# Kernel tuning notes

Hardware: AMD Instinct MI355X
Metric: run time of the kernel (lower is better)

## Reference

```python
import jax, jax.numpy as jnp
import numpy as np

NUM_ITERATIONS = 3  # init kwarg num_iterations
EPS = 1e-12         # F.normalize eps


def _k_means_routing(priors, num_iterations):
    # priors: (B, O, I, J) = (batch, out_capsules, in_capsules, out_length)
    out = priors.mean(axis=-2, keepdims=True)  # (B, O, 1, J)
    for _ in range(num_iterations):
        norm = jnp.sqrt(jnp.sum(out * out, axis=-1, keepdims=True))
        out_n = out / jnp.maximum(norm, EPS)                       # L2 normalize over J
        logits = jnp.sum(priors * out_n, axis=-1, keepdims=True)   # (B, O, I, 1) dot similarity
        coef = jax.nn.softmax(logits, axis=-2)                     # softmax over in_capsules
        out = jnp.sum(coef * priors, axis=-2, keepdims=True)       # (B, O, 1, J)
    return jnp.squeeze(out, axis=-2)  # (B, O, J); squash=False so no squash


def setup_inputs() -> dict:
    key = jax.random.key(0)
    k1, k2 = jax.random.split(key)
    B, I, L = 32, 512, 64   # batch, in_capsules, in_length
    O, J = 128, 64          # out_capsules, out_length
    x = jax.random.normal(k1, (B, I, L), dtype=jnp.float32)
    # xavier_uniform for weight (O, J, L): fan_in = J*L... torch uses size(1)*prod(rest)
    bound = float(np.sqrt(6.0 / (J * L + O * L)))
    weight = jax.random.uniform(k2, (O, J, L), dtype=jnp.float32, minval=-bound, maxval=bound)
    return {"x": x, "weight": weight}


def reference(x, weight):
    # priors[b,o,i,j] = sum_l weight[o,j,l] * x[b,i,l]  -> (B, O, I, J)
    priors = jnp.einsum('ojl,bil->boij', weight, x)
    return _k_means_routing(priors, NUM_ITERATIONS)
```

## Files before the change

### kernel.cpp

```cpp
#include <hip/hip_runtime.h>
#include <hip/hip_fp16.h>


#define CB 32
#define CI 512
#define CL 64
#define CO 128
#define OPB 8
#define NT 1024

typedef _Float16 half8 __attribute__((ext_vector_type(8)));
typedef float f32x4 __attribute__((ext_vector_type(4)));

static __device__ __forceinline__ _Float16 half_sel(uint v, int sh) {
  union { unsigned short s; _Float16 h; } c;
  c.s = (unsigned short)(v >> sh);
  return c.h;
}

__global__ __launch_bounds__(256) void caps_gram(const float* __restrict__ wg,
                                                 __half2* __restrict__ Gq) {
  const int o = blockIdx.x;
  const int h = blockIdx.y;
  const int t = threadIdx.x;
  __shared__ float wl[64 * 65];
#pragma unroll
  for (int k = 0; k < 16; ++k) {
    int f = t + 256 * k;
    int j = f >> 6, l = f & 63;
    wl[j * 65 + l] = wg[(o << 12) + f];
  }
  __syncthreads();
  const int l1 = h * 32 + (t >> 3);
  const int kq = t & 7;
  const int l2b = kq << 3;
  float acc[8];
#pragma unroll
  for (int m = 0; m < 8; ++m) acc[m] = 0.f;
#pragma unroll 4
  for (int j = 0; j < 64; ++j) {
    float wa = wl[j * 65 + l1];
#pragma unroll
    for (int m = 0; m < 8; ++m) acc[m] += wa * wl[j * 65 + l2b + m];
  }
  union { __half2 h2[4]; uint4 u; } pk;
#pragma unroll
  for (int q = 0; q < 4; ++q)
    pk.h2[q] = __floats2half2_rn(acc[2 * q], acc[2 * q + 1]);
  reinterpret_cast<uint4*>(Gq)[(o << 9) + (kq << 6) + l1] = pk.u;
}

__global__ __launch_bounds__(NT)
__attribute__((amdgpu_num_vgpr(64)))
void caps_main(const float* __restrict__ xg,
               const float* __restrict__ wg,
               const __half2* __restrict__ Gq,
               float* __restrict__ outg) {
  const int b = blockIdx.y;
  const int obase = blockIdx.x * OPB;
  const int t = threadIdx.x;
  const int w = t >> 6;
  const int lane = t & 63;
  const int g = lane >> 4;
  const int o15 = lane & 15;
  const int oc = o15 & 7;

  __shared__ __align__(16) _Float16 xs[CI * CL];
  __shared__ __align__(16) _Float16 cfx[OPB * CI];
  __shared__ __align__(16) _Float16 wn16[OPB * CL];
  __shared__ __align__(16) float xc_s[OPB * CL];
  __shared__ float se_part[16 * OPB];
  float* const xcpart = reinterpret_cast<float*>(cfx);
  char* const xs_b = reinterpret_cast<char*>(xs);
  char* const cf_b = reinterpret_cast<char*>(cfx);
  char* const wn_b = reinterpret_cast<char*>(wn16);

  const int qh = w >> 2, nt = w & 3;
  const int lcol = nt * 16 + o15;

  const uint4* Gp = reinterpret_cast<const uint4*>(Gq) +
                    ((obase + (w & 7)) << 9) + lane;
  uint4 ga0, ga1;

  {
    const float4* xg4 = reinterpret_cast<const float4*>(xg + b * (CI * CL));
#pragma unroll
    for (int k = 0; k < 4; ++k) {
      int f = t + NT * k;
      int i = f >> 3, lu = f & 7;
      float4 a = xg4[2 * f];
      float4 c = xg4[2 * f + 1];
      union { _Float16 h[8]; uint4 u; } cv;
      cv.h[0] = (_Float16)a.x; cv.h[1] = (_Float16)a.y;
      cv.h[2] = (_Float16)a.z; cv.h[3] = (_Float16)a.w;
      cv.h[4] = (_Float16)c.x; cv.h[5] = (_Float16)c.y;
      cv.h[6] = (_Float16)c.z; cv.h[7] = (_Float16)c.w;
      int off = ((i >> 4) * 4 + (lu >> 1)) * 512 + (i & 15) * 32 + (lu & 1) * 16;
      *reinterpret_cast<uint4*>(xs_b + off) = cv.u;
    }
  }
  __syncthreads();

  uint4 bt0, bt1, bt2, bt3;
  float xbs = 0.f;
  {
    const uint* xrd32 = reinterpret_cast<const uint*>(
                            xs_b + nt * 512 + ((o15 & 8) << 1)) +
                        ((o15 & 7) >> 1);
    const int sh = (o15 & 1) << 4;
#define GATHW(K, BT)                                                        \
  {                                                                         \
    int P = qh * 16 + (K)*4 + g;                                            \
    const uint* xk = xrd32 + (P >> 1) * 512 + (P & 1) * 64;                 \
    uint d0 = xk[0], d1 = xk[8], d2 = xk[16], d3 = xk[24];                  \
    uint d4 = xk[32], d5 = xk[40], d6 = xk[48], d7 = xk[56];                \
    union { _Float16 h[8]; uint4 u; } fv;                                   \
    fv.h[0] = half_sel(d0, sh); fv.h[1] = half_sel(d1, sh);                 \
    fv.h[2] = half_sel(d2, sh); fv.h[3] = half_sel(d3, sh);                 \
    fv.h[4] = half_sel(d4, sh); fv.h[5] = half_sel(d5, sh);                 \
    fv.h[6] = half_sel(d6, sh); fv.h[7] = half_sel(d7, sh);                 \
    xbs += (float)fv.h[0] + (float)fv.h[1] + (float)fv.h[2] +               \
           (float)fv.h[3] + (float)fv.h[4] + (float)fv.h[5] +               \
           (float)fv.h[6] + (float)fv.h[7];                                 \
    BT = fv.u;                                                              \
  }
    GATHW(0, bt0) GATHW(1, bt1) GATHW(2, bt2) GATHW(3, bt3)
#undef GATHW
    xbs += __shfl_xor(xbs, 16, 64);
    xbs += __shfl_xor(xbs, 32, 64);
    if (g == 0) xcpart[qh * 512 + lcol] = xbs;
    if (w < 8) { ga0 = Gp[0]; ga1 = Gp[64]; }
  }
  __syncthreads();

  for (int pass = 0; pass < 4; ++pass) {
    if (pass > 0) {
      half8 bw0 = *reinterpret_cast<const half8*>(
          wn_b + oc * 128 + ((g ^ oc) << 4));
      half8 bw1 = *reinterpret_cast<const half8*>(
          wn_b + oc * 128 + (((4 + g) ^ oc) << 4));
      float sacc = 0.f;
#pragma unroll
      for (int ti = 0; ti < 2; ++ti) {
        const int st = 2 * w + ti;
        const int itb = st * 2048;
        const int abase = o15 * 32 + ((g & 1) << 4);
        half8 a0 = *reinterpret_cast<const half8*>(
            xs_b + itb + ((g >> 1) * 512) + abase);
        half8 a1 = *reinterpret_cast<const half8*>(
            xs_b + itb + ((2 + (g >> 1)) * 512) + abase);
        f32x4 d = {0.f, 0.f, 0.f, 0.f};
        d = __builtin_amdgcn_mfma_f32_16x16x32_f16(a0, bw0, d, 0, 0, 0);
        d = __builtin_amdgcn_mfma_f32_16x16x32_f16(a1, bw1, d, 0, 0, 0);
        float e0 = __expf(d[0]), e1 = __expf(d[1]);
        float e2 = __expf(d[2]), e3 = __expf(d[3]);
        sacc += (e0 + e1) + (e2 + e3);
        if (o15 < 8) {
          int p = st * 2 + (g >> 1);
          union { _Float16 h[4]; uint2 u; } pk;
          pk.h[0] = (_Float16)e0; pk.h[1] = (_Float16)e1;
          pk.h[2] = (_Float16)e2; pk.h[3] = (_Float16)e3;
          *reinterpret_cast<uint2*>(cf_b + o15 * 1024 + ((p ^ o15) << 4) +
                                    ((g & 1) << 3)) = pk.u;
        }
      }
      if (pass == 3) {
        sacc += __shfl_xor(sacc, 16, 64);
        sacc += __shfl_xor(sacc, 32, 64);
        if (lane < 8) se_part[w * 8 + lane] = sacc;
      }
      __syncthreads();

      if (w < 8 && pass < 3) { ga0 = Gp[0]; ga1 = Gp[64]; }
      f32x4 d = {0.f, 0.f, 0.f, 0.f};
#define MFMAK(K, BT)                                                        \
  {                                                                         \
    int p = qh * 16 + (K)*4 + g;                                            \
    half8 a = *reinterpret_cast<const half8*>(cf_b + oc * 1024 +            \
                                              ((p ^ oc) << 4));             \
    d = __builtin_amdgcn_mfma_f32_16x16x32_f16(                             \
        a, *reinterpret_cast<const half8*>(&BT), d, 0, 0, 0);               \
  }
      MFMAK(0, bt0) MFMAK(1, bt1) MFMAK(2, bt2) MFMAK(3, bt3)
#undef MFMAK
      __syncthreads();
      if (g < 2) {
#pragma unroll
        for (int r = 0; r < 4; ++r)
          xcpart[qh * 512 + (g * 4 + r) * 64 + lcol] = d[r];
      }
      __syncthreads();
    }

    if (w < 8) {
      float sxc;
      if (pass == 0) {
        sxc = xcpart[lane] + xcpart[512 + lane] + xcpart[1024 + lane] +
              xcpart[1536 + lane];
      } else {
        sxc = xcpart[w * 64 + lane] + xcpart[512 + w * 64 + lane] +
              xcpart[1024 + w * 64 + lane] + xcpart[1536 + w * 64 + lane];
      }
      float xcv;
      if (pass == 3) {
        float sp = se_part[(lane & 15) * 8 + w];
        sp += __shfl_xor(sp, 1, 64);
        sp += __shfl_xor(sp, 2, 64);
        sp += __shfl_xor(sp, 4, 64);
        sp += __shfl_xor(sp, 8, 64);
        xcv = sxc / sp;
      } else {
        xcv = sxc;
      }
      xc_s[(w << 6) + lane] = xcv;
      if (pass < 3) {
        const float4* xc4 = reinterpret_cast<const float4*>(&xc_s[w << 6]);
        float u0 = 0.f, u1 = 0.f, u2 = 0.f, u3 = 0.f;
#define GDOT(V, K)                                                          \
  {                                                                         \
    float4 xa = xc4[2 * (K)], xb = xc4[2 * (K) + 1];                        \
    float2 h0 = __half22float2(*reinterpret_cast<const __half2*>(&V.x));    \
    float2 h1 = __half22float2(*reinterpret_cast<const __half2*>(&V.y));    \
    float2 h2 = __half22float2(*reinterpret_cast<const __half2*>(&V.z));    \
    float2 h3 = __half22float2(*reinterpret_cast<const __half2*>(&V.w));    \
    u0 += h0.x * xa.x; u1 += h0.y * xa.y;                                   \
    u2 += h1.x * xa.z; u3 += h1.y * xa.w;                                   \
    u0 += h2.x * xb.x; u1 += h2.y * xb.y;                                   \
    u2 += h3.x * xb.z; u3 += h3.y * xb.w;                                   \
  }
        uint4 gb0 = Gp[128], gb1 = Gp[192];
        GDOT(ga0, 0) GDOT(ga1, 1)
        ga0 = Gp[256]; ga1 = Gp[320];
        GDOT(gb0, 2) GDOT(gb1, 3)
        gb0 = Gp[384]; gb1 = Gp[448];
        GDOT(ga0, 4) GDOT(ga1, 5)
        GDOT(gb0, 6) GDOT(gb1, 7)
#undef GDOT
        float uv = (u0 + u1) + (u2 + u3);
        float sq = uv * xcv;
#pragma unroll
        for (int m = 32; m; m >>= 1) sq += __shfl_xor(sq, m, 64);
        float wnv = uv / fmaxf(sqrtf(fmaxf(sq, 0.f)), 1e-12f);
        union { _Float16 hf; unsigned short us; } wc;
        wc.hf = (_Float16)wnv;
        *reinterpret_cast<unsigned short*>(
            wn_b + w * 128 + (((lane >> 3) ^ w) << 4) + ((lane & 7) << 1)) =
            wc.us;
      }
    }
    __syncthreads();
  }

  if (w < 8) {
    const float* Wp = wg + ((((obase + w) << 6) + lane) << 6);
    float a0 = 0.f, a1 = 0.f, a2 = 0.f, a3 = 0.f;
#pragma unroll
    for (int k = 0; k < 16; ++k) {
      float4 wv = *reinterpret_cast<const float4*>(&Wp[k << 2]);
      float4 xv = *reinterpret_cast<const float4*>(&xc_s[(w << 6) + (k << 2)]);
      a0 += wv.x * xv.x; a1 += wv.y * xv.y;
      a2 += wv.z * xv.z; a3 += wv.w * xv.w;
    }
    outg[((b << 7) + obase + w) * 64 + lane] = (a0 + a1) + (a2 + a3);
  }
}

extern "C" void kernel_launch(void* const* d_in, const int* in_sizes, int n_in,
                              void* d_out, int out_size, void* d_ws, size_t ws_size,
                              hipStream_t stream) {
  const float* x = (const float*)d_in[0];
  const float* wgt = (const float*)d_in[1];
  float* out = (float*)d_out;
  __half2* Gq = (__half2*)d_ws;

  caps_gram<<<dim3(CO, 2), dim3(256), 0, stream>>>(wgt, Gq);
  caps_main<<<dim3(CO / OPB, CB), dim3(NT), 0, stream>>>(x, wgt, Gq, out);
}
```

Measured before the change: 40.07 us.

## Halve block to 512 threads, double per-wave work, give xcpart own LDS

The main kernel now runs 8 waves instead of 16, so each wave does twice the MFMA and softmax tiles and holds 8 B-fragments in registers, under a VGPR limit raised to 128. All waves now take part in the per-capsule normalize and output phases, which removes the idle-half branches. The partial-sum buffer moves into its own LDS array instead of aliasing the coefficient buffer, which removes one barrier per pass. The cost is less thread-level parallelism per block and higher register pressure.

```diff
diff --git a/kernel.cpp b/kernel.cpp
--- a/kernel.cpp
+++ b/kernel.cpp
@@ -7,7 +7,7 @@
 #define CL 64
 #define CO 128
 #define OPB 8
-#define NT 1024
+#define NT 512
 
 typedef _Float16 half8 __attribute__((ext_vector_type(8)));
 typedef float f32x4 __attribute__((ext_vector_type(4)));
@@ -51,7 +51,7 @@
 }
 
 __global__ __launch_bounds__(NT)
-__attribute__((amdgpu_num_vgpr(64)))
+__attribute__((amdgpu_num_vgpr(128)))
 void caps_main(const float* __restrict__ xg,
                const float* __restrict__ wg,
                const __half2* __restrict__ Gq,
@@ -66,26 +66,26 @@
   const int oc = o15 & 7;
 
   __shared__ __align__(16) _Float16 xs[CI * CL];
-  __shared__ __align__(16) _Float16 cfx[OPB * CI];
+  __shared__ __align__(16) _Float16 coefT[OPB * CI];
+  __shared__ __align__(16) float xcpart[2 * OPB * CL];
   __shared__ __align__(16) _Float16 wn16[OPB * CL];
   __shared__ __align__(16) float xc_s[OPB * CL];
-  __shared__ float se_part[16 * OPB];
-  float* const xcpart = reinterpret_cast<float*>(cfx);
+  __shared__ float se_part[OPB * OPB];
   char* const xs_b = reinterpret_cast<char*>(xs);
-  char* const cf_b = reinterpret_cast<char*>(cfx);
+  char* const cf_b = reinterpret_cast<char*>(coefT);
   char* const wn_b = reinterpret_cast<char*>(wn16);
 
-  const int qh = w >> 2, nt = w & 3;
+  const int kh = w >> 2, nt = w & 3;
   const int lcol = nt * 16 + o15;
 
   const uint4* Gp = reinterpret_cast<const uint4*>(Gq) +
-                    ((obase + (w & 7)) << 9) + lane;
+                    ((obase + w) << 9) + lane;
   uint4 ga0, ga1;
 
   {
     const float4* xg4 = reinterpret_cast<const float4*>(xg + b * (CI * CL));
 #pragma unroll
-    for (int k = 0; k < 4; ++k) {
+    for (int k = 0; k < 8; ++k) {
       int f = t + NT * k;
       int i = f >> 3, lu = f & 7;
       float4 a = xg4[2 * f];
@@ -101,16 +101,16 @@
   }
   __syncthreads();
 
-  uint4 bt0, bt1, bt2, bt3;
-  float xbs = 0.f;
+  uint4 bt0, bt1, bt2, bt3, bt4, bt5, bt6, bt7;
   {
     const uint* xrd32 = reinterpret_cast<const uint*>(
                             xs_b + nt * 512 + ((o15 & 8) << 1)) +
                         ((o15 & 7) >> 1);
     const int sh = (o15 & 1) << 4;
+    float xbs = 0.f;
 #define GATHW(K, BT)                                                        \
   {                                                                         \
-    int P = qh * 16 + (K)*4 + g;                                            \
+    int P = kh * 32 + (K)*4 + g;                                            \
     const uint* xk = xrd32 + (P >> 1) * 512 + (P & 1) * 64;                 \
     uint d0 = xk[0], d1 = xk[8], d2 = xk[16], d3 = xk[24];                  \
     uint d4 = xk[32], d5 = xk[40], d6 = xk[48], d7 = xk[56];                \
@@ -125,11 +125,12 @@
     BT = fv.u;                                                              \
   }
     GATHW(0, bt0) GATHW(1, bt1) GATHW(2, bt2) GATHW(3, bt3)
+    GATHW(4, bt4) GATHW(5, bt5) GATHW(6, bt6) GATHW(7, bt7)
 #undef GATHW
     xbs += __shfl_xor(xbs, 16, 64);
     xbs += __shfl_xor(xbs, 32, 64);
-    if (g == 0) xcpart[qh * 512 + lcol] = xbs;
-    if (w < 8) { ga0 = Gp[0]; ga1 = Gp[64]; }
+    if (g == 0) xcpart[kh * 512 + lcol] = xbs;
+    ga0 = Gp[0]; ga1 = Gp[64];
   }
   __syncthreads();
 
@@ -141,8 +142,8 @@
           wn_b + oc * 128 + (((4 + g) ^ oc) << 4));
       float sacc = 0.f;
 #pragma unroll
-      for (int ti = 0; ti < 2; ++ti) {
-        const int st = 2 * w + ti;
+      for (int ti = 0; ti < 4; ++ti) {
+        const int st = 4 * w + ti;
         const int itb = st * 2048;
         const int abase = o15 * 32 + ((g & 1) << 4);
         half8 a0 = *reinterpret_cast<const half8*>(
@@ -171,43 +172,40 @@
       }
       __syncthreads();
 
-      if (w < 8 && pass < 3) { ga0 = Gp[0]; ga1 = Gp[64]; }
+      if (pass < 3) { ga0 = Gp[0]; ga1 = Gp[64]; }
       f32x4 d = {0.f, 0.f, 0.f, 0.f};
 #define MFMAK(K, BT)                                                        \
   {                                                                         \
-    int p = qh * 16 + (K)*4 + g;                                            \
+    int p = kh * 32 + (K)*4 + g;                                            \
     half8 a = *reinterpret_cast<const half8*>(cf_b + oc * 1024 +            \
                                               ((p ^ oc) << 4));             \
     d = __builtin_amdgcn_mfma_f32_16x16x32_f16(                             \
         a, *reinterpret_cast<const half8*>(&BT), d, 0, 0, 0);               \
   }
       MFMAK(0, bt0) MFMAK(1, bt1) MFMAK(2, bt2) MFMAK(3, bt3)
+      MFMAK(4, bt4) MFMAK(5, bt5) MFMAK(6, bt6) MFMAK(7, bt7)
 #undef MFMAK
+      if (g < 2) {
+#pragma unroll
+        for (int r = 0; r < 4; ++r)
+          xcpart[kh * 512 + (g * 4 + r) * 64 + lcol] = d[r];
+      }
       __syncthreads();
-      if (g < 2) {
-#pragma unroll
-        for (int r = 0; r < 4; ++r)
-          xcpart[qh * 512 + (g * 4 + r) * 64 + lcol] = d[r];
-      }
-      __syncthreads();
-    }
-
-    if (w < 8) {
+    }
+
+    {
       float sxc;
       if (pass == 0) {
-        sxc = xcpart[lane] + xcpart[512 + lane] + xcpart[1024 + lane] +
-              xcpart[1536 + lane];
+        sxc = xcpart[lane] + xcpart[512 + lane];
       } else {
-        sxc = xcpart[w * 64 + lane] + xcpart[512 + w * 64 + lane] +
-              xcpart[1024 + w * 64 + lane] + xcpart[1536 + w * 64 + lane];
+        sxc = xcpart[w * 64 + lane] + xcpart[512 + w * 64 + lane];
       }
       float xcv;
       if (pass == 3) {
-        float sp = se_part[(lane & 15) * 8 + w];
+        float sp = se_part[(lane & 7) * 8 + w];
         sp += __shfl_xor(sp, 1, 64);
         sp += __shfl_xor(sp, 2, 64);
         sp += __shfl_xor(sp, 4, 64);
-        sp += __shfl_xor(sp, 8, 64);
         xcv = sxc / sp;
       } else {
         xcv = sxc;
@@ -251,7 +249,7 @@
     __syncthreads();
   }
 
-  if (w < 8) {
+  {
     const float* Wp = wg + ((((obase + w) << 6) + lane) << 6);
     float a0 = 0.f, a1 = 0.f, a2 = 0.f, a3 = 0.f;
 #pragma unroll
```

New measurement: 39.73 us. About the same (-0.8%).
